# Kernel tuning notes

Hardware: AMD Instinct MI355X
Metric: run time of the kernel (lower is better)

Reference implementation:

```python
import jax, jax.numpy as jnp
import numpy as np

N_NODES = 100000
N_EDGES = 1600000
NFEAT = 256
NHID = 128


def setup_inputs() -> dict:
    key = jax.random.key(0)
    k1, k2, k3, k4, k5 = jax.random.split(key, 5)
    x = jax.random.normal(k1, (N_NODES, NFEAT), dtype=jnp.float32)
    edge_src = jax.random.randint(k2, (N_EDGES,), 0, N_NODES, dtype=jnp.int64)
    edge_dst = jax.random.randint(k3, (N_EDGES,), 0, N_NODES, dtype=jnp.int64)
    edge_w = jax.random.uniform(k4, (N_EDGES,), dtype=jnp.float32)
    W = jax.random.normal(k5, (NFEAT, NHID), dtype=jnp.float32) * (1.0 / np.sqrt(NFEAT))
    b = jnp.zeros((NHID,), dtype=jnp.float32)
    return {"x": x, "edge_src": edge_src, "edge_dst": edge_dst, "edge_w": edge_w, "W": W, "b": b}


def reference(x, edge_src, edge_dst, edge_w, W, b):
    # GraphConvolution: support = x @ W ; out = spmm(adj, support) + b ; then ReLU
    support = x @ W                                  # [N, nhid]
    msgs = support[edge_src] * edge_w[:, None]       # [E, nhid] gather + scale
    agg = jax.ops.segment_sum(msgs, edge_dst, num_segments=N_NODES)  # [N, nhid]
    return jax.nn.relu(agg + b)
```

## Files before the change

### kernel.cpp

```cpp
#include <hip/hip_runtime.h>
#include <hip/hip_bf16.h>

#define NFEAT 256
#define NHID  128
#define NPB   128
#define BMAX  2048
#define SCHUNK 2048

typedef short s16x8 __attribute__((ext_vector_type(8)));
typedef float f32x4 __attribute__((ext_vector_type(4)));
typedef float f32x2 __attribute__((ext_vector_type(2)));

static __device__ __forceinline__ ushort bfbits(float f) {
  __hip_bfloat16 h = __float2bfloat16(f);
  return *reinterpret_cast<ushort*>(&h);
}

__global__ __launch_bounds__(256) void prep_kernel(
    const float* __restrict__ W, ushort* __restrict__ Wt,
    const int* __restrict__ edst, int* __restrict__ histT,
    int n_edges, int B, int G) {
  __shared__ int hist[BMAX];
  if (blockIdx.x < 128) {
    const int id = blockIdx.x * 256 + threadIdx.x;
    const int k = id >> 7, n = id & 127;
    Wt[n * NFEAT + k] = bfbits(W[id]);
    return;
  }
  const int g = blockIdx.x - 128;
  for (int b = threadIdx.x; b < B; b += 256) hist[b] = 0;
  __syncthreads();
  const int e0 = g * SCHUNK;
  const int e1 = (e0 + SCHUNK < n_edges) ? e0 + SCHUNK : n_edges;
  for (int e = e0 + threadIdx.x; e < e1; e += 256)
    atomicAdd(&hist[(uint)edst[e] >> 7], 1);
  __syncthreads();
  for (int b = threadIdx.x; b < B; b += 256) histT[(size_t)b * G + g] = hist[b];
}

__global__ __launch_bounds__(256) void scan1_kernel(
    const int* __restrict__ in, int* __restrict__ exc,
    int* __restrict__ bsums, int n) {
  const int tid = threadIdx.x;
  const int lane = tid & 63, wid = tid >> 6;
  const int base = blockIdx.x * 1024 + tid * 4;
  int v0 = 0, v1 = 0, v2 = 0, v3 = 0;
  if (base + 3 < n) {
    int4 v = *(const int4*)(in + base);
    v0 = v.x; v1 = v.y; v2 = v.z; v3 = v.w;
  } else {
    if (base + 0 < n) v0 = in[base + 0];
    if (base + 1 < n) v1 = in[base + 1];
    if (base + 2 < n) v2 = in[base + 2];
  }
  const int tsum = v0 + v1 + v2 + v3;
  int t = tsum;
#pragma unroll
  for (int d = 1; d < 64; d <<= 1) {
    int u = __shfl_up(t, d);
    if (lane >= d) t += u;
  }
  __shared__ int wtot[4], wpre[4];
  if (lane == 63) wtot[wid] = t;
  __syncthreads();
  if (tid == 0) {
    int s = 0;
    for (int w = 0; w < 4; ++w) { wpre[w] = s; s += wtot[w]; }
    bsums[blockIdx.x] = s;
  }
  __syncthreads();
  const int off = (t - tsum) + wpre[wid];
  if (base + 0 < n) exc[base + 0] = off;
  if (base + 1 < n) exc[base + 1] = off + v0;
  if (base + 2 < n) exc[base + 2] = off + v0 + v1;
  if (base + 3 < n) exc[base + 3] = off + v0 + v1 + v2;
}

__global__ __launch_bounds__(256) void scan2_kernel(int* __restrict__ bsums, int nb) {
  __shared__ int wtot[4], wpre[4], tot_s;
  const int tid = threadIdx.x;
  const int lane = tid & 63, wid = tid >> 6;
  int carry = 0;
  for (int base = 0; base < nb; base += 256) {
    const int idx = base + tid;
    const int v = (idx < nb) ? bsums[idx] : 0;
    int t = v;
#pragma unroll
    for (int d = 1; d < 64; d <<= 1) {
      int u = __shfl_up(t, d);
      if (lane >= d) t += u;
    }
    if (lane == 63) wtot[wid] = t;
    __syncthreads();
    if (tid == 0) {
      int s = 0;
      for (int w = 0; w < 4; ++w) { wpre[w] = s; s += wtot[w]; }
      tot_s = s;
    }
    __syncthreads();
    if (idx < nb) bsums[idx] = carry + (t - v) + wpre[wid];
    carry += tot_s;
    __syncthreads();
  }
}

__global__ __launch_bounds__(256) void scan3_kernel(
    const int* __restrict__ exc, const int* __restrict__ bsums,
    int* __restrict__ baseT, int* __restrict__ bucket_start,
    int n, int G, int B, int n_edges) {
  const int i = blockIdx.x * 256 + threadIdx.x;
  if (i < n) {
    const int v = exc[i] + bsums[i >> 10];
    const int b = i / G, g = i % G;
    baseT[(size_t)g * B + b] = v;
    if (g == 0) bucket_start[b] = v;
  }
  if (i == 0) bucket_start[B] = n_edges;
}

__global__ __launch_bounds__(256) void gemm_scatter_fused(
    const float* __restrict__ x, const ushort* __restrict__ Wt,
    ushort* __restrict__ sup, int n_nodes,
    const int* __restrict__ esrc, const int* __restrict__ edst,
    const float* __restrict__ ew, const int* __restrict__ baseT,
    int2* __restrict__ packed2, int n_edges, int B, int G, int n_gemm) {
  __shared__ ushort As[64 * 64];
  __shared__ ushort Bs[128 * 64];

  const int idx = blockIdx.x;
  const long long total = (long long)n_gemm + G;
  const int c_lo = (int)((long long)idx * G / total);
  const int c_hi = (int)(((long long)idx + 1) * G / total);
  int role, sub;
  if (c_hi > c_lo) { role = 0; sub = c_lo; }
  else             { role = 1; sub = idx - c_hi; }

  if (role == 0) {
    int* cursor = (int*)As;
    const int g = sub;
    for (int b = threadIdx.x; b < B; b += 256) cursor[b] = baseT[(size_t)g * B + b];
    __syncthreads();
    const int e0 = g * SCHUNK;
    if (e0 + SCHUNK <= n_edges) {
      int d[8], s[8]; float w[8];
#pragma unroll
      for (int j = 0; j < 8; ++j) {
        const int e = e0 + j * 256 + threadIdx.x;
        d[j] = edst[e]; s[j] = esrc[e]; w[j] = ew[e];
      }
#pragma unroll
      for (int j = 0; j < 8; ++j) {
        const int pos = atomicAdd(&cursor[(uint)d[j] >> 7], 1);
        packed2[pos] = make_int2(s[j] | ((d[j] & (NPB - 1)) << 18), __float_as_int(w[j]));
      }
    } else {
      const int e1 = n_edges;
      for (int e = e0 + threadIdx.x; e < e1; e += 256) {
        const int dst = edst[e];
        const int pos = atomicAdd(&cursor[(uint)dst >> 7], 1);
        packed2[pos] = make_int2(esrc[e] | ((dst & (NPB - 1)) << 18), __float_as_int(ew[e]));
      }
    }
    return;
  }

  const int t = threadIdx.x;
  const int wid = t >> 6;
  const int lane = t & 63;
  const int rowBase = sub * 64;
  if (rowBase >= n_nodes) return;

  f32x4 acc[4][2];
#pragma unroll
  for (int m = 0; m < 4; ++m)
#pragma unroll
    for (int n = 0; n < 2; ++n) acc[m][n] = (f32x4){0.f, 0.f, 0.f, 0.f};

  const float4* x4 = (const float4*)x;

  for (int kc = 0; kc < 4; ++kc) {
    __syncthreads();
#pragma unroll
    for (int it = 0; it < 4; ++it) {
      const int i4 = t + it * 256;
      const int r = i4 >> 4, k4 = i4 & 15;
      const int row = rowBase + r;
      float4 v = make_float4(0.f, 0.f, 0.f, 0.f);
      if (row < n_nodes) v = x4[(size_t)row * (NFEAT / 4) + kc * 16 + k4];
      ushort4 h;
      h.x = bfbits(v.x); h.y = bfbits(v.y); h.z = bfbits(v.z); h.w = bfbits(v.w);
      int byte = (r << 7) + (k4 << 3);
      byte ^= (r & 7) << 4;
      *(ushort4*)((char*)As + byte) = h;
    }
#pragma unroll
    for (int it = 0; it < 8; ++it) {
      const int i2 = t + it * 256;
      const int col = i2 >> 4, k4 = i2 & 15;
      const ushort4 h = *(const ushort4*)(Wt + col * NFEAT + kc * 64 + k4 * 4);
      int byte = (col << 7) + (k4 << 3);
      byte ^= (col & 7) << 4;
      *(ushort4*)((char*)Bs + byte) = h;
    }
    __syncthreads();
#pragma unroll
    for (int ks = 0; ks < 2; ++ks) {
      const int k0 = ks * 32 + (lane >> 4) * 8;
      s16x8 af[4], bfr[2];
#pragma unroll
      for (int m = 0; m < 4; ++m) {
        const int r = m * 16 + (lane & 15);
        int byte = (r << 7) + (k0 << 1);
        byte ^= (r & 7) << 4;
        af[m] = *(const s16x8*)((const char*)As + byte);
      }
#pragma unroll
      for (int n = 0; n < 2; ++n) {
        const int c = wid * 32 + n * 16 + (lane & 15);
        int byte = (c << 7) + (k0 << 1);
        byte ^= (c & 7) << 4;
        bfr[n] = *(const s16x8*)((const char*)Bs + byte);
      }
#pragma unroll
      for (int m = 0; m < 4; ++m)
#pragma unroll
        for (int n = 0; n < 2; ++n)
          acc[m][n] = __builtin_amdgcn_mfma_f32_16x16x32_bf16(af[m], bfr[n], acc[m][n], 0, 0, 0);
    }
  }

#pragma unroll
  for (int m = 0; m < 4; ++m) {
#pragma unroll
    for (int rr = 0; rr < 4; ++rr) {
      const int row = rowBase + m * 16 + (lane >> 4) * 4 + rr;
      if (row < n_nodes) {
#pragma unroll
        for (int n = 0; n < 2; ++n) {
          const int col = wid * 32 + n * 16 + (lane & 15);
          sup[(size_t)row * NHID + col] = bfbits(acc[m][n][rr]);
        }
      }
    }
  }
}

__global__ __launch_bounds__(256) void bucket_build_kernel(
    const int2* __restrict__ packed2, const int* __restrict__ bucket_start,
    int2* __restrict__ packedN, int* __restrict__ row_start,
    int n_nodes, int n_edges) {
  __shared__ int cnt[NPB];
  __shared__ int st[NPB];
  __shared__ int cur[NPB];
  __shared__ int w0tot;
  const int tid = threadIdx.x;
  const int b = blockIdx.x;
  const int s0 = bucket_start[b];
  const int s1 = bucket_start[b + 1];
  const int m = s1 - s0;

  if (tid < NPB) cnt[tid] = 0;
  __syncthreads();

  for (int i = tid; i < m; i += 256)
    atomicAdd(&cnt[((uint)packed2[s0 + i].x >> 18) & (NPB - 1)], 1);
  __syncthreads();

  {
    const int v = (tid < NPB) ? cnt[tid] : 0;
    int t = v;
#pragma unroll
    for (int d = 1; d < 64; d <<= 1) {
      int u = __shfl_up(t, d);
      if ((tid & 63) >= d) t += u;
    }
    if (tid == 63) w0tot = t;
    __syncthreads();
    if (tid < NPB) {
      const int s = (t - v) + ((tid >= 64) ? w0tot : 0);
      st[tid] = s;
      cur[tid] = s;
    }
    __syncthreads();
  }

  for (int i = tid; i < m; i += 256) {
    const int2 e = packed2[s0 + i];
    const int dl = ((uint)e.x >> 18) & (NPB - 1);
    const int pos = atomicAdd(&cur[dl], 1);
    packedN[s0 + pos] = e;
  }

  if (tid < NPB) {
    const int node = b * NPB + tid;
    if (node < n_nodes) row_start[node] = s0 + st[tid];
  }
  if (b == 0 && tid == 0) row_start[n_nodes] = n_edges;
}

__global__ __launch_bounds__(256) void agg_kernel(
    const ushort* __restrict__ sup, const int2* __restrict__ packed,
    const int* __restrict__ row_start, const float* __restrict__ bias,
    float* __restrict__ out, int n_nodes) {
  const int node = blockIdx.x * 4 + (threadIdx.x >> 6);
  if (node >= n_nodes) return;
  const int lane = threadIdx.x & 63;
  const int start = __builtin_amdgcn_readfirstlane(row_start[node]);
  const int end   = __builtin_amdgcn_readfirstlane(row_start[node + 1]);

  float a0 = 0.f, a1 = 0.f, b0 = 0.f, b1 = 0.f;
  float c0 = 0.f, c1 = 0.f, d0 = 0.f, d1 = 0.f;
  int i = start;
  for (; i + 7 < end; i += 8) {
    const int2 e0 = packed[i + 0];
    const int2 e1 = packed[i + 1];
    const int2 e2 = packed[i + 2];
    const int2 e3 = packed[i + 3];
    const int2 e4 = packed[i + 4];
    const int2 e5 = packed[i + 5];
    const int2 e6 = packed[i + 6];
    const int2 e7 = packed[i + 7];
    const uint u0 = *(const uint*)(sup + ((size_t)((uint)e0.x & 0x3FFFFu) << 7) + lane * 2);
    const uint u1 = *(const uint*)(sup + ((size_t)((uint)e1.x & 0x3FFFFu) << 7) + lane * 2);
    const uint u2 = *(const uint*)(sup + ((size_t)((uint)e2.x & 0x3FFFFu) << 7) + lane * 2);
    const uint u3 = *(const uint*)(sup + ((size_t)((uint)e3.x & 0x3FFFFu) << 7) + lane * 2);
    const uint u4 = *(const uint*)(sup + ((size_t)((uint)e4.x & 0x3FFFFu) << 7) + lane * 2);
    const uint u5 = *(const uint*)(sup + ((size_t)((uint)e5.x & 0x3FFFFu) << 7) + lane * 2);
    const uint u6 = *(const uint*)(sup + ((size_t)((uint)e6.x & 0x3FFFFu) << 7) + lane * 2);
    const uint u7 = *(const uint*)(sup + ((size_t)((uint)e7.x & 0x3FFFFu) << 7) + lane * 2);
    const float w0 = __int_as_float(e0.y), w1 = __int_as_float(e1.y);
    const float w2 = __int_as_float(e2.y), w3 = __int_as_float(e3.y);
    const float w4 = __int_as_float(e4.y), w5 = __int_as_float(e5.y);
    const float w6 = __int_as_float(e6.y), w7 = __int_as_float(e7.y);
    a0 += __uint_as_float(u0 << 16) * w0 + __uint_as_float(u4 << 16) * w4;
    a1 += __uint_as_float(u0 & 0xffff0000u) * w0 + __uint_as_float(u4 & 0xffff0000u) * w4;
    b0 += __uint_as_float(u1 << 16) * w1 + __uint_as_float(u5 << 16) * w5;
    b1 += __uint_as_float(u1 & 0xffff0000u) * w1 + __uint_as_float(u5 & 0xffff0000u) * w5;
    c0 += __uint_as_float(u2 << 16) * w2 + __uint_as_float(u6 << 16) * w6;
    c1 += __uint_as_float(u2 & 0xffff0000u) * w2 + __uint_as_float(u6 & 0xffff0000u) * w6;
    d0 += __uint_as_float(u3 << 16) * w3 + __uint_as_float(u7 << 16) * w7;
    d1 += __uint_as_float(u3 & 0xffff0000u) * w3 + __uint_as_float(u7 & 0xffff0000u) * w7;
  }
  for (; i + 3 < end; i += 4) {
    const int2 e0 = packed[i + 0];
    const int2 e1 = packed[i + 1];
    const int2 e2 = packed[i + 2];
    const int2 e3 = packed[i + 3];
    const uint u0 = *(const uint*)(sup + ((size_t)((uint)e0.x & 0x3FFFFu) << 7) + lane * 2);
    const uint u1 = *(const uint*)(sup + ((size_t)((uint)e1.x & 0x3FFFFu) << 7) + lane * 2);
    const uint u2 = *(const uint*)(sup + ((size_t)((uint)e2.x & 0x3FFFFu) << 7) + lane * 2);
    const uint u3 = *(const uint*)(sup + ((size_t)((uint)e3.x & 0x3FFFFu) << 7) + lane * 2);
    const float w0 = __int_as_float(e0.y), w1 = __int_as_float(e1.y);
    const float w2 = __int_as_float(e2.y), w3 = __int_as_float(e3.y);
    a0 += __uint_as_float(u0 << 16) * w0 + __uint_as_float(u2 << 16) * w2;
    a1 += __uint_as_float(u0 & 0xffff0000u) * w0 + __uint_as_float(u2 & 0xffff0000u) * w2;
    b0 += __uint_as_float(u1 << 16) * w1 + __uint_as_float(u3 << 16) * w3;
    b1 += __uint_as_float(u1 & 0xffff0000u) * w1 + __uint_as_float(u3 & 0xffff0000u) * w3;
  }
  for (; i < end; ++i) {
    const int2 e0 = packed[i];
    const uint u0 = *(const uint*)(sup + ((size_t)((uint)e0.x & 0x3FFFFu) << 7) + lane * 2);
    const float w0 = __int_as_float(e0.y);
    a0 += __uint_as_float(u0 << 16) * w0;
    a1 += __uint_as_float(u0 & 0xffff0000u) * w0;
  }

  const float2 bb = ((const float2*)bias)[lane];
  f32x2 r;
  r.x = fmaxf((a0 + b0) + (c0 + d0) + bb.x, 0.f);
  r.y = fmaxf((a1 + b1) + (c1 + d1) + bb.y, 0.f);
  __builtin_nontemporal_store(r, (f32x2*)out + (size_t)node * (NHID / 2) + lane);
}

__global__ __launch_bounds__(256) void scatter_bf16_kernel(
    const ushort* __restrict__ sup, const int* __restrict__ esrc,
    const int* __restrict__ edst, const float* __restrict__ ew,
    float* __restrict__ out, int n_edges) {
  const long long idx = (long long)blockIdx.x * 256 + threadIdx.x;
  const int e = (int)(idx >> 6);
  const int c2 = (int)(idx & 63);
  if (e >= n_edges) return;
  const int s = esrc[e];
  const int d = edst[e];
  const float wt = ew[e];
  const uint u = *(const uint*)(sup + (size_t)s * NHID + c2 * 2);
  float* drow = out + (size_t)d * NHID + c2 * 2;
  atomicAdd(drow + 0, __uint_as_float(u << 16) * wt);
  atomicAdd(drow + 1, __uint_as_float(u & 0xffff0000u) * wt);
}

__global__ __launch_bounds__(256) void bias_relu_kernel(
    float* __restrict__ out, const float* __restrict__ b, int n4) {
  const int i = blockIdx.x * 256 + threadIdx.x;
  if (i >= n4) return;
  float4 v = ((float4*)out)[i];
  const float4 bb = ((const float4*)b)[i & (NHID / 4 - 1)];
  v.x = fmaxf(v.x + bb.x, 0.f);
  v.y = fmaxf(v.y + bb.y, 0.f);
  v.z = fmaxf(v.z + bb.z, 0.f);
  v.w = fmaxf(v.w + bb.w, 0.f);
  ((float4*)out)[i] = v;
}

static inline size_t align_up(size_t v, size_t a) { return (v + a - 1) & ~(a - 1); }

extern "C" void kernel_launch(void* const* d_in, const int* in_sizes, int n_in,
                              void* d_out, int out_size, void* d_ws, size_t ws_size,
                              hipStream_t stream) {
  const float* x    = (const float*)d_in[0];
  const int*   esrc = (const int*)d_in[1];
  const int*   edst = (const int*)d_in[2];
  const float* ew   = (const float*)d_in[3];
  const float* W    = (const float*)d_in[4];
  const float* b    = (const float*)d_in[5];
  float* out = (float*)d_out;

  const int n_nodes = in_sizes[0] / NFEAT;
  const int n_edges = in_sizes[1];

  const int B = (n_nodes + NPB - 1) / NPB;
  const int G = (n_edges + SCHUNK - 1) / SCHUNK;
  const long long n_scan_ll = (long long)B * G;

  char* ws = (char*)d_ws;
  size_t off = 0;
  ushort* sup       = (ushort*)(ws + off); off = align_up(off + (size_t)n_nodes * NHID * 2, 256);
  ushort* Wt        = (ushort*)(ws + off); off = align_up(off + (size_t)NFEAT * NHID * 2, 256);
  int* histT        = (int*)(ws + off);    off = align_up(off + (size_t)B * G * 4, 256);
  int* exc          = (int*)(ws + off);    off = align_up(off + (size_t)B * G * 4, 256);
  int* baseT        = (int*)(ws + off);    off = align_up(off + (size_t)B * G * 4, 256);
  int* bsums        = (int*)(ws + off);    off = align_up(off + 1024 * 4, 256);
  int* bucket_start = (int*)(ws + off);    off = align_up(off + ((size_t)B + 1) * 4, 256);
  int* row_start    = (int*)(ws + off);    off = align_up(off + ((size_t)n_nodes + 1) * 4, 256);
  int2* packed2     = (int2*)(ws + off);   off = align_up(off + (size_t)n_edges * 8, 256);
  int2* packedN     = (int2*)(ws + off);   off = align_up(off + (size_t)n_edges * 8, 256);
  const bool csr_ok = (off <= ws_size) && (n_nodes <= 256 * 1024) && (B <= BMAX) &&
                      (n_scan_ll <= 1024 * 1024);

  const int n_gemm = (n_nodes + 63) / 64;

  if (csr_ok) {
    prep_kernel<<<128 + G, 256, 0, stream>>>(W, Wt, edst, histT, n_edges, B, G);

    const int n_scan = (int)n_scan_ll;
    const int nb = (n_scan + 1023) / 1024;
    scan1_kernel<<<nb, 256, 0, stream>>>(histT, exc, bsums, n_scan);
    scan2_kernel<<<1, 256, 0, stream>>>(bsums, nb);
    scan3_kernel<<<(n_scan + 255) / 256, 256, 0, stream>>>(exc, bsums, baseT, bucket_start, n_scan, G, B, n_edges);

    gemm_scatter_fused<<<n_gemm + G, 256, 0, stream>>>(
        x, Wt, sup, n_nodes, esrc, edst, ew, baseT, packed2, n_edges, B, G, n_gemm);

    bucket_build_kernel<<<B, 256, 0, stream>>>(
        packed2, bucket_start, packedN, row_start, n_nodes, n_edges);

    agg_kernel<<<(n_nodes + 3) / 4, 256, 0, stream>>>(sup, packedN, row_start, b, out, n_nodes);
  } else {
    prep_kernel<<<128, 256, 0, stream>>>(W, Wt, edst, (int*)d_ws, 0, 1, 1);
    gemm_scatter_fused<<<n_gemm, 256, 0, stream>>>(
        x, Wt, sup, n_nodes, esrc, edst, ew, (int*)d_ws, (int2*)d_ws,
        0, 1, 0, n_gemm);
    hipMemsetAsync(out, 0, (size_t)n_nodes * NHID * sizeof(float), stream);
    const long long threads = (long long)n_edges * 64;
    scatter_bf16_kernel<<<(int)((threads + 255) / 256), 256, 0, stream>>>(sup, esrc, edst, ew, out, n_edges);
    const int n4 = n_nodes * NHID / 4;
    bias_relu_kernel<<<(n4 + 255) / 256, 256, 0, stream>>>(out, b, n4);
  }
}
```

Baseline: 139.2 us.

## Prefetch GEMM tiles into registers and split agg wave into two edge halves

The GEMM loop now loads the next k-chunk of x and Wt into registers while MFMAs run on the current chunk, so global loads overlap with compute. The barriers are rearranged to suit this, with the end-of-iteration sync moved after the MFMAs. The aggregation kernel splits each 64-lane wave into two halves that handle alternate edges with 8-byte loads per lane, then combines the halves with a cross-half shuffle. This aims at more bytes in flight per gather and fewer loop iterations, at the cost of more registers and a shuffle-reduce step.

```diff
diff --git a/kernel.cpp b/kernel.cpp
--- a/kernel.cpp
+++ b/kernel.cpp
@@ -177,18 +177,32 @@
     for (int n = 0; n < 2; ++n) acc[m][n] = (f32x4){0.f, 0.f, 0.f, 0.f};
 
   const float4* x4 = (const float4*)x;
+  float4 va[4];
+  ushort4 vb[8];
+
+#pragma unroll
+  for (int it = 0; it < 4; ++it) {
+    const int i4 = t + it * 256;
+    const int r = i4 >> 4, k4 = i4 & 15;
+    const int row = rowBase + r;
+    va[it] = (row < n_nodes) ? x4[(size_t)row * (NFEAT / 4) + k4]
+                             : make_float4(0.f, 0.f, 0.f, 0.f);
+  }
+#pragma unroll
+  for (int it = 0; it < 8; ++it) {
+    const int i2 = t + it * 256;
+    const int col = i2 >> 4, k4 = i2 & 15;
+    vb[it] = *(const ushort4*)(Wt + col * NFEAT + k4 * 4);
+  }
 
   for (int kc = 0; kc < 4; ++kc) {
-    __syncthreads();
 #pragma unroll
     for (int it = 0; it < 4; ++it) {
       const int i4 = t + it * 256;
       const int r = i4 >> 4, k4 = i4 & 15;
-      const int row = rowBase + r;
-      float4 v = make_float4(0.f, 0.f, 0.f, 0.f);
-      if (row < n_nodes) v = x4[(size_t)row * (NFEAT / 4) + kc * 16 + k4];
       ushort4 h;
-      h.x = bfbits(v.x); h.y = bfbits(v.y); h.z = bfbits(v.z); h.w = bfbits(v.w);
+      h.x = bfbits(va[it].x); h.y = bfbits(va[it].y);
+      h.z = bfbits(va[it].z); h.w = bfbits(va[it].w);
       int byte = (r << 7) + (k4 << 3);
       byte ^= (r & 7) << 4;
       *(ushort4*)((char*)As + byte) = h;
@@ -197,12 +211,29 @@
     for (int it = 0; it < 8; ++it) {
       const int i2 = t + it * 256;
       const int col = i2 >> 4, k4 = i2 & 15;
-      const ushort4 h = *(const ushort4*)(Wt + col * NFEAT + kc * 64 + k4 * 4);
       int byte = (col << 7) + (k4 << 3);
       byte ^= (col & 7) << 4;
-      *(ushort4*)((char*)Bs + byte) = h;
-    }
-    __syncthreads();
+      *(ushort4*)((char*)Bs + byte) = vb[it];
+    }
+    __syncthreads();
+
+    if (kc < 3) {
+#pragma unroll
+      for (int it = 0; it < 4; ++it) {
+        const int i4 = t + it * 256;
+        const int r = i4 >> 4, k4 = i4 & 15;
+        const int row = rowBase + r;
+        va[it] = (row < n_nodes) ? x4[(size_t)row * (NFEAT / 4) + (kc + 1) * 16 + k4]
+                                 : make_float4(0.f, 0.f, 0.f, 0.f);
+      }
+#pragma unroll
+      for (int it = 0; it < 8; ++it) {
+        const int i2 = t + it * 256;
+        const int col = i2 >> 4, k4 = i2 & 15;
+        vb[it] = *(const ushort4*)(Wt + col * NFEAT + (kc + 1) * 64 + k4 * 4);
+      }
+    }
+
 #pragma unroll
     for (int ks = 0; ks < 2; ++ks) {
       const int k0 = ks * 32 + (lane >> 4) * 8;
@@ -227,6 +258,7 @@
         for (int n = 0; n < 2; ++n)
           acc[m][n] = __builtin_amdgcn_mfma_f32_16x16x32_bf16(af[m], bfr[n], acc[m][n], 0, 0, 0);
     }
+    __syncthreads();
   }
 
 #pragma unroll
@@ -305,71 +337,88 @@
   const int node = blockIdx.x * 4 + (threadIdx.x >> 6);
   if (node >= n_nodes) return;
   const int lane = threadIdx.x & 63;
+  const int half = lane >> 5;
+  const int c4 = lane & 31;
   const int start = __builtin_amdgcn_readfirstlane(row_start[node]);
   const int end   = __builtin_amdgcn_readfirstlane(row_start[node + 1]);
 
-  float a0 = 0.f, a1 = 0.f, b0 = 0.f, b1 = 0.f;
-  float c0 = 0.f, c1 = 0.f, d0 = 0.f, d1 = 0.f;
+  float a0 = 0.f, a1 = 0.f, a2 = 0.f, a3 = 0.f;
+  float b0 = 0.f, b1 = 0.f, b2 = 0.f, b3 = 0.f;
+
   int i = start;
+  for (; i + 15 < end; i += 16) {
+    int2 pe[16];
+#pragma unroll
+    for (int j = 0; j < 16; ++j) pe[j] = packed[i + j];
+    uint2 u[8]; float w[8];
+#pragma unroll
+    for (int s = 0; s < 8; ++s) {
+      const int ex = half ? pe[2 * s + 1].x : pe[2 * s].x;
+      w[s] = __int_as_float(half ? pe[2 * s + 1].y : pe[2 * s].y);
+      u[s] = *(const uint2*)(sup + ((size_t)((uint)ex & 0x3FFFFu) << 7) + c4 * 4);
+    }
+#pragma unroll
+    for (int s = 0; s < 8; s += 2) {
+      a0 += __uint_as_float(u[s].x << 16) * w[s];
+      a1 += __uint_as_float(u[s].x & 0xffff0000u) * w[s];
+      a2 += __uint_as_float(u[s].y << 16) * w[s];
+      a3 += __uint_as_float(u[s].y & 0xffff0000u) * w[s];
+      b0 += __uint_as_float(u[s + 1].x << 16) * w[s + 1];
+      b1 += __uint_as_float(u[s + 1].x & 0xffff0000u) * w[s + 1];
+      b2 += __uint_as_float(u[s + 1].y << 16) * w[s + 1];
+      b3 += __uint_as_float(u[s + 1].y & 0xffff0000u) * w[s + 1];
+    }
+  }
   for (; i + 7 < end; i += 8) {
-    const int2 e0 = packed[i + 0];
-    const int2 e1 = packed[i + 1];
-    const int2 e2 = packed[i + 2];
-    const int2 e3 = packed[i + 3];
-    const int2 e4 = packed[i + 4];
-    const int2 e5 = packed[i + 5];
-    const int2 e6 = packed[i + 6];
-    const int2 e7 = packed[i + 7];
-    const uint u0 = *(const uint*)(sup + ((size_t)((uint)e0.x & 0x3FFFFu) << 7) + lane * 2);
-    const uint u1 = *(const uint*)(sup + ((size_t)((uint)e1.x & 0x3FFFFu) << 7) + lane * 2);
-    const uint u2 = *(const uint*)(sup + ((size_t)((uint)e2.x & 0x3FFFFu) << 7) + lane * 2);
-    const uint u3 = *(const uint*)(sup + ((size_t)((uint)e3.x & 0x3FFFFu) << 7) + lane * 2);
-    const uint u4 = *(const uint*)(sup + ((size_t)((uint)e4.x & 0x3FFFFu) << 7) + lane * 2);
-    const uint u5 = *(const uint*)(sup + ((size_t)((uint)e5.x & 0x3FFFFu) << 7) + lane * 2);
-    const uint u6 = *(const uint*)(sup + ((size_t)((uint)e6.x & 0x3FFFFu) << 7) + lane * 2);
-    const uint u7 = *(const uint*)(sup + ((size_t)((uint)e7.x & 0x3FFFFu) << 7) + lane * 2);
-    const float w0 = __int_as_float(e0.y), w1 = __int_as_float(e1.y);
-    const float w2 = __int_as_float(e2.y), w3 = __int_as_float(e3.y);
-    const float w4 = __int_as_float(e4.y), w5 = __int_as_float(e5.y);
-    const float w6 = __int_as_float(e6.y), w7 = __int_as_float(e7.y);
-    a0 += __uint_as_float(u0 << 16) * w0 + __uint_as_float(u4 << 16) * w4;
-    a1 += __uint_as_float(u0 & 0xffff0000u) * w0 + __uint_as_float(u4 & 0xffff0000u) * w4;
-    b0 += __uint_as_float(u1 << 16) * w1 + __uint_as_float(u5 << 16) * w5;
-    b1 += __uint_as_float(u1 & 0xffff0000u) * w1 + __uint_as_float(u5 & 0xffff0000u) * w5;
-    c0 += __uint_as_float(u2 << 16) * w2 + __uint_as_float(u6 << 16) * w6;
-    c1 += __uint_as_float(u2 & 0xffff0000u) * w2 + __uint_as_float(u6 & 0xffff0000u) * w6;
-    d0 += __uint_as_float(u3 << 16) * w3 + __uint_as_float(u7 << 16) * w7;
-    d1 += __uint_as_float(u3 & 0xffff0000u) * w3 + __uint_as_float(u7 & 0xffff0000u) * w7;
-  }
-  for (; i + 3 < end; i += 4) {
-    const int2 e0 = packed[i + 0];
-    const int2 e1 = packed[i + 1];
-    const int2 e2 = packed[i + 2];
-    const int2 e3 = packed[i + 3];
-    const uint u0 = *(const uint*)(sup + ((size_t)((uint)e0.x & 0x3FFFFu) << 7) + lane * 2);
-    const uint u1 = *(const uint*)(sup + ((size_t)((uint)e1.x & 0x3FFFFu) << 7) + lane * 2);
-    const uint u2 = *(const uint*)(sup + ((size_t)((uint)e2.x & 0x3FFFFu) << 7) + lane * 2);
-    const uint u3 = *(const uint*)(sup + ((size_t)((uint)e3.x & 0x3FFFFu) << 7) + lane * 2);
-    const float w0 = __int_as_float(e0.y), w1 = __int_as_float(e1.y);
-    const float w2 = __int_as_float(e2.y), w3 = __int_as_float(e3.y);
-    a0 += __uint_as_float(u0 << 16) * w0 + __uint_as_float(u2 << 16) * w2;
-    a1 += __uint_as_float(u0 & 0xffff0000u) * w0 + __uint_as_float(u2 & 0xffff0000u) * w2;
-    b0 += __uint_as_float(u1 << 16) * w1 + __uint_as_float(u3 << 16) * w3;
-    b1 += __uint_as_float(u1 & 0xffff0000u) * w1 + __uint_as_float(u3 & 0xffff0000u) * w3;
-  }
-  for (; i < end; ++i) {
-    const int2 e0 = packed[i];
-    const uint u0 = *(const uint*)(sup + ((size_t)((uint)e0.x & 0x3FFFFu) << 7) + lane * 2);
-    const float w0 = __int_as_float(e0.y);
-    a0 += __uint_as_float(u0 << 16) * w0;
-    a1 += __uint_as_float(u0 & 0xffff0000u) * w0;
-  }
-
-  const float2 bb = ((const float2*)bias)[lane];
-  f32x2 r;
-  r.x = fmaxf((a0 + b0) + (c0 + d0) + bb.x, 0.f);
-  r.y = fmaxf((a1 + b1) + (c1 + d1) + bb.y, 0.f);
-  __builtin_nontemporal_store(r, (f32x2*)out + (size_t)node * (NHID / 2) + lane);
+    int2 pe[8];
+#pragma unroll
+    for (int j = 0; j < 8; ++j) pe[j] = packed[i + j];
+    uint2 u[4]; float w[4];
+#pragma unroll
+    for (int s = 0; s < 4; ++s) {
+      const int ex = half ? pe[2 * s + 1].x : pe[2 * s].x;
+      w[s] = __int_as_float(half ? pe[2 * s + 1].y : pe[2 * s].y);
+      u[s] = *(const uint2*)(sup + ((size_t)((uint)ex & 0x3FFFFu) << 7) + c4 * 4);
+    }
+#pragma unroll
+    for (int s = 0; s < 4; s += 2) {
+      a0 += __uint_as_float(u[s].x << 16) * w[s];
+      a1 += __uint_as_float(u[s].x & 0xffff0000u) * w[s];
+      a2 += __uint_as_float(u[s].y << 16) * w[s];
+      a3 += __uint_as_float(u[s].y & 0xffff0000u) * w[s];
+      b0 += __uint_as_float(u[s + 1].x << 16) * w[s + 1];
+      b1 += __uint_as_float(u[s + 1].x & 0xffff0000u) * w[s + 1];
+      b2 += __uint_as_float(u[s + 1].y << 16) * w[s + 1];
+      b3 += __uint_as_float(u[s + 1].y & 0xffff0000u) * w[s + 1];
+    }
+  }
+  for (; i < end; i += 2) {
+    const int2 p0 = packed[i];
+    const int2 p1 = (i + 1 < end) ? packed[i + 1] : make_int2(0, 0);
+    const int ex = half ? p1.x : p0.x;
+    const float wv = __int_as_float(half ? p1.y : p0.y);
+    const uint2 uu = *(const uint2*)(sup + ((size_t)((uint)ex & 0x3FFFFu) << 7) + c4 * 4);
+    a0 += __uint_as_float(uu.x << 16) * wv;
+    a1 += __uint_as_float(uu.x & 0xffff0000u) * wv;
+    a2 += __uint_as_float(uu.y << 16) * wv;
+    a3 += __uint_as_float(uu.y & 0xffff0000u) * wv;
+  }
+
+  float s0 = a0 + b0, s1 = a1 + b1, s2 = a2 + b2, s3 = a3 + b3;
+  s0 += __shfl_xor(s0, 32);
+  s1 += __shfl_xor(s1, 32);
+  s2 += __shfl_xor(s2, 32);
+  s3 += __shfl_xor(s3, 32);
+
+  if (half == 0) {
+    const float4 bb = ((const float4*)bias)[c4];
+    f32x4 r;
+    r.x = fmaxf(s0 + bb.x, 0.f);
+    r.y = fmaxf(s1 + bb.y, 0.f);
+    r.z = fmaxf(s2 + bb.z, 0.f);
+    r.w = fmaxf(s3 + bb.w, 0.f);
+    __builtin_nontemporal_store(r, (f32x4*)out + (size_t)node * 32 + c4);
+  }
 }
 
 __global__ __launch_bounds__(256) void scatter_bf16_kernel(
```

Result: slower. 226.9 us (+63.0%).

## Split GEMM tiles across scatter and bucket-build kernels to overlap work

Applied to the files above, without the earlier changes.

Moves the GEMM tile body into a shared device helper and splits the GEMM row tiles in half. One half runs alongside the edge scatter kernel and the other half runs inside the bucket-build kernel, interleaved by block index. The aim is to balance the two phases so the latency-bound bucket build is co-scheduled with compute-heavy GEMM tiles. In exchange, the bucket-build blocks now carry larger shared memory for the GEMM staging buffers, which may lower their occupancy.

```diff
diff --git a/kernel.cpp b/kernel.cpp
--- a/kernel.cpp
+++ b/kernel.cpp
@@ -14,6 +14,90 @@
 static __device__ __forceinline__ ushort bfbits(float f) {
   __hip_bfloat16 h = __float2bfloat16(f);
   return *reinterpret_cast<ushort*>(&h);
+}
+
+__device__ __forceinline__ void gemm_tile(
+    const float* __restrict__ x, const ushort* __restrict__ Wt,
+    ushort* __restrict__ sup, int n_nodes, int rowBase,
+    ushort* As, ushort* Bs) {
+  const int t = threadIdx.x;
+  const int wid = t >> 6;
+  const int lane = t & 63;
+  if (rowBase >= n_nodes) return;
+
+  f32x4 acc[4][2];
+#pragma unroll
+  for (int m = 0; m < 4; ++m)
+#pragma unroll
+    for (int n = 0; n < 2; ++n) acc[m][n] = (f32x4){0.f, 0.f, 0.f, 0.f};
+
+  const float4* x4 = (const float4*)x;
+
+  for (int kc = 0; kc < 4; ++kc) {
+    __syncthreads();
+#pragma unroll
+    for (int it = 0; it < 4; ++it) {
+      const int i4 = t + it * 256;
+      const int r = i4 >> 4, k4 = i4 & 15;
+      const int row = rowBase + r;
+      float4 v = make_float4(0.f, 0.f, 0.f, 0.f);
+      if (row < n_nodes) v = x4[(size_t)row * (NFEAT / 4) + kc * 16 + k4];
+      ushort4 h;
+      h.x = bfbits(v.x); h.y = bfbits(v.y); h.z = bfbits(v.z); h.w = bfbits(v.w);
+      int byte = (r << 7) + (k4 << 3);
+      byte ^= (r & 7) << 4;
+      *(ushort4*)((char*)As + byte) = h;
+    }
+#pragma unroll
+    for (int it = 0; it < 8; ++it) {
+      const int i2 = t + it * 256;
+      const int col = i2 >> 4, k4 = i2 & 15;
+      const ushort4 h = *(const ushort4*)(Wt + col * NFEAT + kc * 64 + k4 * 4);
+      int byte = (col << 7) + (k4 << 3);
+      byte ^= (col & 7) << 4;
+      *(ushort4*)((char*)Bs + byte) = h;
+    }
+    __syncthreads();
+#pragma unroll
+    for (int ks = 0; ks < 2; ++ks) {
+      const int k0 = ks * 32 + (lane >> 4) * 8;
+      s16x8 af[4], bfr[2];
+#pragma unroll
+      for (int m = 0; m < 4; ++m) {
+        const int r = m * 16 + (lane & 15);
+        int byte = (r << 7) + (k0 << 1);
+        byte ^= (r & 7) << 4;
+        af[m] = *(const s16x8*)((const char*)As + byte);
+      }
+#pragma unroll
+      for (int n = 0; n < 2; ++n) {
+        const int c = wid * 32 + n * 16 + (lane & 15);
+        int byte = (c << 7) + (k0 << 1);
+        byte ^= (c & 7) << 4;
+        bfr[n] = *(const s16x8*)((const char*)Bs + byte);
+      }
+#pragma unroll
+      for (int m = 0; m < 4; ++m)
+#pragma unroll
+        for (int n = 0; n < 2; ++n)
+          acc[m][n] = __builtin_amdgcn_mfma_f32_16x16x32_bf16(af[m], bfr[n], acc[m][n], 0, 0, 0);
+    }
+  }
+
+#pragma unroll
+  for (int m = 0; m < 4; ++m) {
+#pragma unroll
+    for (int rr = 0; rr < 4; ++rr) {
+      const int row = rowBase + m * 16 + (lane >> 4) * 4 + rr;
+      if (row < n_nodes) {
+#pragma unroll
+        for (int n = 0; n < 2; ++n) {
+          const int col = wid * 32 + n * 16 + (lane & 15);
+          sup[(size_t)row * NHID + col] = bfbits(acc[m][n][rr]);
+        }
+      }
+    }
+  }
 }
 
 __global__ __launch_bounds__(256) void prep_kernel(
@@ -118,17 +202,17 @@
   if (i == 0) bucket_start[B] = n_edges;
 }
 
-__global__ __launch_bounds__(256) void gemm_scatter_fused(
+__global__ __launch_bounds__(256) void fusedA_kernel(
     const float* __restrict__ x, const ushort* __restrict__ Wt,
     ushort* __restrict__ sup, int n_nodes,
     const int* __restrict__ esrc, const int* __restrict__ edst,
     const float* __restrict__ ew, const int* __restrict__ baseT,
-    int2* __restrict__ packed2, int n_edges, int B, int G, int n_gemm) {
+    int2* __restrict__ packed2, int n_edges, int B, int G, int nA) {
   __shared__ ushort As[64 * 64];
   __shared__ ushort Bs[128 * 64];
 
   const int idx = blockIdx.x;
-  const long long total = (long long)n_gemm + G;
+  const long long total = (long long)nA + G;
   const int c_lo = (int)((long long)idx * G / total);
   const int c_hi = (int)(((long long)idx + 1) * G / total);
   int role, sub;
@@ -154,8 +238,7 @@
         packed2[pos] = make_int2(s[j] | ((d[j] & (NPB - 1)) << 18), __float_as_int(w[j]));
       }
     } else {
-      const int e1 = n_edges;
-      for (int e = e0 + threadIdx.x; e < e1; e += 256) {
+      for (int e = e0 + threadIdx.x; e < n_edges; e += 256) {
         const int dst = edst[e];
         const int pos = atomicAdd(&cursor[(uint)dst >> 7], 1);
         packed2[pos] = make_int2(esrc[e] | ((dst & (NPB - 1)) << 18), __float_as_int(ew[e]));
@@ -164,138 +247,78 @@
     return;
   }
 
-  const int t = threadIdx.x;
-  const int wid = t >> 6;
-  const int lane = t & 63;
-  const int rowBase = sub * 64;
-  if (rowBase >= n_nodes) return;
-
-  f32x4 acc[4][2];
-#pragma unroll
-  for (int m = 0; m < 4; ++m)
-#pragma unroll
-    for (int n = 0; n < 2; ++n) acc[m][n] = (f32x4){0.f, 0.f, 0.f, 0.f};
-
-  const float4* x4 = (const float4*)x;
-
-  for (int kc = 0; kc < 4; ++kc) {
-    __syncthreads();
-#pragma unroll
-    for (int it = 0; it < 4; ++it) {
-      const int i4 = t + it * 256;
-      const int r = i4 >> 4, k4 = i4 & 15;
-      const int row = rowBase + r;
-      float4 v = make_float4(0.f, 0.f, 0.f, 0.f);
-      if (row < n_nodes) v = x4[(size_t)row * (NFEAT / 4) + kc * 16 + k4];
-      ushort4 h;
-      h.x = bfbits(v.x); h.y = bfbits(v.y); h.z = bfbits(v.z); h.w = bfbits(v.w);
-      int byte = (r << 7) + (k4 << 3);
-      byte ^= (r & 7) << 4;
-      *(ushort4*)((char*)As + byte) = h;
-    }
-#pragma unroll
-    for (int it = 0; it < 8; ++it) {
-      const int i2 = t + it * 256;
-      const int col = i2 >> 4, k4 = i2 & 15;
-      const ushort4 h = *(const ushort4*)(Wt + col * NFEAT + kc * 64 + k4 * 4);
-      int byte = (col << 7) + (k4 << 3);
-      byte ^= (col & 7) << 4;
-      *(ushort4*)((char*)Bs + byte) = h;
-    }
-    __syncthreads();
-#pragma unroll
-    for (int ks = 0; ks < 2; ++ks) {
-      const int k0 = ks * 32 + (lane >> 4) * 8;
-      s16x8 af[4], bfr[2];
-#pragma unroll
-      for (int m = 0; m < 4; ++m) {
-        const int r = m * 16 + (lane & 15);
-        int byte = (r << 7) + (k0 << 1);
-        byte ^= (r & 7) << 4;
-        af[m] = *(const s16x8*)((const char*)As + byte);
-      }
-#pragma unroll
-      for (int n = 0; n < 2; ++n) {
-        const int c = wid * 32 + n * 16 + (lane & 15);
-        int byte = (c << 7) + (k0 << 1);
-        byte ^= (c & 7) << 4;
-        bfr[n] = *(const s16x8*)((const char*)Bs + byte);
-      }
-#pragma unroll
-      for (int m = 0; m < 4; ++m)
-#pragma unroll
-        for (int n = 0; n < 2; ++n)
-          acc[m][n] = __builtin_amdgcn_mfma_f32_16x16x32_bf16(af[m], bfr[n], acc[m][n], 0, 0, 0);
-    }
-  }
-
-#pragma unroll
-  for (int m = 0; m < 4; ++m) {
-#pragma unroll
-    for (int rr = 0; rr < 4; ++rr) {
-      const int row = rowBase + m * 16 + (lane >> 4) * 4 + rr;
-      if (row < n_nodes) {
-#pragma unroll
-        for (int n = 0; n < 2; ++n) {
-          const int col = wid * 32 + n * 16 + (lane & 15);
-          sup[(size_t)row * NHID + col] = bfbits(acc[m][n][rr]);
-        }
-      }
-    }
-  }
-}
-
-__global__ __launch_bounds__(256) void bucket_build_kernel(
+  gemm_tile(x, Wt, sup, n_nodes, sub * 64, As, Bs);
+}
+
+__global__ __launch_bounds__(256) void fusedB_kernel(
+    const float* __restrict__ x, const ushort* __restrict__ Wt,
+    ushort* __restrict__ sup, int n_nodes,
     const int2* __restrict__ packed2, const int* __restrict__ bucket_start,
     int2* __restrict__ packedN, int* __restrict__ row_start,
-    int n_nodes, int n_edges) {
+    int n_edges, int B, int nB, int gemm_base) {
+  __shared__ ushort As[64 * 64];
+  __shared__ ushort Bs[128 * 64];
   __shared__ int cnt[NPB];
   __shared__ int st[NPB];
   __shared__ int cur[NPB];
   __shared__ int w0tot;
-  const int tid = threadIdx.x;
-  const int b = blockIdx.x;
-  const int s0 = bucket_start[b];
-  const int s1 = bucket_start[b + 1];
-  const int m = s1 - s0;
-
-  if (tid < NPB) cnt[tid] = 0;
-  __syncthreads();
-
-  for (int i = tid; i < m; i += 256)
-    atomicAdd(&cnt[((uint)packed2[s0 + i].x >> 18) & (NPB - 1)], 1);
-  __syncthreads();
-
-  {
-    const int v = (tid < NPB) ? cnt[tid] : 0;
-    int t = v;
-#pragma unroll
-    for (int d = 1; d < 64; d <<= 1) {
-      int u = __shfl_up(t, d);
-      if ((tid & 63) >= d) t += u;
-    }
-    if (tid == 63) w0tot = t;
-    __syncthreads();
+
+  const int idx = blockIdx.x;
+  const long long total = (long long)nB + B;
+  const int c_lo = (int)((long long)idx * B / total);
+  const int c_hi = (int)(((long long)idx + 1) * B / total);
+  int role, sub;
+  if (c_hi > c_lo) { role = 0; sub = c_lo; }
+  else             { role = 1; sub = idx - c_hi; }
+
+  if (role == 0) {
+    const int tid = threadIdx.x;
+    const int b = sub;
+    const int s0 = bucket_start[b];
+    const int s1 = bucket_start[b + 1];
+    const int m = s1 - s0;
+
+    if (tid < NPB) cnt[tid] = 0;
+    __syncthreads();
+
+    for (int i = tid; i < m; i += 256)
+      atomicAdd(&cnt[((uint)packed2[s0 + i].x >> 18) & (NPB - 1)], 1);
+    __syncthreads();
+
+    {
+      const int v = (tid < NPB) ? cnt[tid] : 0;
+      int t = v;
+#pragma unroll
+      for (int d = 1; d < 64; d <<= 1) {
+        int u = __shfl_up(t, d);
+        if ((tid & 63) >= d) t += u;
+      }
+      if (tid == 63) w0tot = t;
+      __syncthreads();
+      if (tid < NPB) {
+        const int s = (t - v) + ((tid >= 64) ? w0tot : 0);
+        st[tid] = s;
+        cur[tid] = s;
+      }
+      __syncthreads();
+    }
+
+    for (int i = tid; i < m; i += 256) {
+      const int2 e = packed2[s0 + i];
+      const int dl = ((uint)e.x >> 18) & (NPB - 1);
+      const int pos = atomicAdd(&cur[dl], 1);
+      packedN[s0 + pos] = e;
+    }
+
     if (tid < NPB) {
-      const int s = (t - v) + ((tid >= 64) ? w0tot : 0);
-      st[tid] = s;
-      cur[tid] = s;
-    }
-    __syncthreads();
-  }
-
-  for (int i = tid; i < m; i += 256) {
-    const int2 e = packed2[s0 + i];
-    const int dl = ((uint)e.x >> 18) & (NPB - 1);
-    const int pos = atomicAdd(&cur[dl], 1);
-    packedN[s0 + pos] = e;
-  }
-
-  if (tid < NPB) {
-    const int node = b * NPB + tid;
-    if (node < n_nodes) row_start[node] = s0 + st[tid];
-  }
-  if (b == 0 && tid == 0) row_start[n_nodes] = n_edges;
+      const int node = b * NPB + tid;
+      if (node < n_nodes) row_start[node] = s0 + st[tid];
+    }
+    if (b == 0 && tid == 0) row_start[n_nodes] = n_edges;
+    return;
+  }
+
+  gemm_tile(x, Wt, sup, n_nodes, (gemm_base + sub) * 64, As, Bs);
 }
 
 __global__ __launch_bounds__(256) void agg_kernel(
@@ -438,6 +461,8 @@
                       (n_scan_ll <= 1024 * 1024);
 
   const int n_gemm = (n_nodes + 63) / 64;
+  const int nA = (n_gemm + 1) / 2;
+  const int nB = n_gemm - nA;
 
   if (csr_ok) {
     prep_kernel<<<128 + G, 256, 0, stream>>>(W, Wt, edst, histT, n_edges, B, G);
@@ -448,16 +473,17 @@
     scan2_kernel<<<1, 256, 0, stream>>>(bsums, nb);
     scan3_kernel<<<(n_scan + 255) / 256, 256, 0, stream>>>(exc, bsums, baseT, bucket_start, n_scan, G, B, n_edges);
 
-    gemm_scatter_fused<<<n_gemm + G, 256, 0, stream>>>(
-        x, Wt, sup, n_nodes, esrc, edst, ew, baseT, packed2, n_edges, B, G, n_gemm);
-
-    bucket_build_kernel<<<B, 256, 0, stream>>>(
-        packed2, bucket_start, packedN, row_start, n_nodes, n_edges);
+    fusedA_kernel<<<nA + G, 256, 0, stream>>>(
+        x, Wt, sup, n_nodes, esrc, edst, ew, baseT, packed2, n_edges, B, G, nA);
+
+    fusedB_kernel<<<nB + B, 256, 0, stream>>>(
+        x, Wt, sup, n_nodes, packed2, bucket_start, packedN, row_start,
+        n_edges, B, nB, nA);
 
     agg_kernel<<<(n_nodes + 3) / 4, 256, 0, stream>>>(sup, packedN, row_start, b, out, n_nodes);
   } else {
     prep_kernel<<<128, 256, 0, stream>>>(W, Wt, edst, (int*)d_ws, 0, 1, 1);
-    gemm_scatter_fused<<<n_gemm, 256, 0, stream>>>(
+    fusedA_kernel<<<n_gemm, 256, 0, stream>>>(
         x, Wt, sup, n_nodes, esrc, edst, ew, (int*)d_ws, (int2*)d_ws,
         0, 1, 0, n_gemm);
     hipMemsetAsync(out, 0, (size_t)n_nodes * NHID * sizeof(float), stream);
```

Result: slower. 142.7 us (+2.5%).
